# Optimization experiments

Measured on AMD Instinct MI355X. Metric: run time of the kernel, lower is better.

Reference implementation:

```python
import jax, jax.numpy as jnp
import numpy as np

N, D, E = 50000, 128, 640000


def setup_inputs() -> dict:
    key = jax.random.key(0)
    ks = jax.random.split(key, 8)
    x = jax.random.normal(ks[0], (N, D), dtype=jnp.float32)
    coord = jax.random.normal(ks[1], (N, 3), dtype=jnp.float32)
    edge_index = jax.random.randint(ks[2], (2, E), 0, N, dtype=jnp.int64)
    s = 1.0 / np.sqrt(D)
    W_edge = jax.random.normal(ks[3], (1, D), dtype=jnp.float32)
    b_edge = jnp.zeros((D,), dtype=jnp.float32)
    W1 = jax.random.normal(ks[4], (2 * D, D), dtype=jnp.float32) * s
    b1 = jnp.zeros((D,), dtype=jnp.float32)
    W2 = jax.random.normal(ks[5], (D, D), dtype=jnp.float32) * s
    b2 = jnp.zeros((D,), dtype=jnp.float32)
    return {"x": x, "coord": coord, "edge_index": edge_index,
            "W_edge": W_edge, "b_edge": b_edge,
            "W1": W1, "b1": b1, "W2": W2, "b2": b2}


def reference(x, coord, edge_index, W_edge, b_edge, W1, b1, W2, b2):
    row, col = edge_index[0], edge_index[1]
    dx = coord[row] - coord[col]                      # [E, 3]
    dist = jnp.linalg.norm(dx, axis=-1, keepdims=True)  # [E, 1]
    edge_attr = dist @ W_edge + b_edge                # [E, D]
    edge_msg = jnp.concatenate([x[col], edge_attr], axis=-1)  # [E, 2D]
    h = jax.nn.relu(edge_msg @ W1 + b1)               # [E, D]
    msg = h @ W2 + b2                                 # [E, D]
    agg = jax.ops.segment_sum(msg, row, num_segments=x.shape[0])  # [N, D]
    return x + agg
```

## Files before the change

kernel.cpp:

```cpp
#include <hip/hip_runtime.h>
#include <hip/hip_fp16.h>
#include <hip/hip_bf16.h>
#include <math.h>

#define D 128
#define LDAP 136
#define CAP 64
#define OVMAX 1024

typedef unsigned int   u32;
typedef unsigned short u16;
using f32x4 = __attribute__((ext_vector_type(4))) float;
using s16x8 = __attribute__((ext_vector_type(8))) short;
using u32x4 = __attribute__((ext_vector_type(4))) unsigned int;

__device__ __forceinline__ u16 f2bf(float f) {
    u32 u = __float_as_uint(f);
    return (u16)((u + 0x7FFFu + ((u >> 16) & 1u)) >> 16);
}

__device__ __forceinline__ bool detect_is64(const int* __restrict__ idx32, int E) {
    int lane = threadIdx.x & 63;
    int hi = 0;
    if (lane < E) hi = idx32[2 * lane + 1];
    return __ballot(hi != 0) == 0ull;
}

__global__ __launch_bounds__(128) void prep_zero_kernel(
    const float* __restrict__ W_edge, const float* __restrict__ b_edge,
    const float* __restrict__ W1, const float* __restrict__ b1,
    const float* __restrict__ W2, float* __restrict__ wc,
    u16* __restrict__ Wt1, u16* __restrict__ Wt2,
    u32x4* __restrict__ counts4, int nz4, u32* __restrict__ ovCount)
{
    const int b = blockIdx.x, t = threadIdx.x;
    if (b < D) {
        Wt1[b * D + t] = f2bf(W1[(size_t)t * D + b]);
        Wt2[b * D + t] = f2bf(W2[(size_t)t * D + b]);
    } else if (b == D) {
        if (t == 0) *ovCount = 0u;
        float w = 0.f, c = 0.f;
        #pragma unroll 8
        for (int k = 0; k < D; ++k) {
            float w1 = W1[(size_t)(D + k) * D + t];
            w = fmaf(W_edge[k], w1, w);
            c = fmaf(b_edge[k], w1, c);
        }
        wc[t]     = w;
        wc[D + t] = c + b1[t];
    } else {
        int i = (b - D - 1) * 128 + t;
        if (i < nz4) counts4[i] = (u32x4){0u, 0u, 0u, 0u};
    }
}

__global__ __launch_bounds__(256) void count_direct_kernel(
    const void* __restrict__ eidx, const float* __restrict__ coord,
    u32* __restrict__ counts, u32* __restrict__ packed,
    u32* __restrict__ ovCount, u32* __restrict__ ovRow,
    u32* __restrict__ ovRec, int E)
{
    const bool is64 = detect_is64((const int*)eidx, E);
    const long long* e64 = (const long long*)eidx;
    const int*       e32 = (const int*)eidx;
    const int e = blockIdx.x * 256 + threadIdx.x;
    if (e >= E) return;

    int row, col;
    if (is64) { row = (int)e64[e]; col = (int)e64[E + e]; }
    else      { row = e32[e];      col = e32[E + e];      }

    u32 seq = atomicAdd(&counts[row], 1u);

    float dx = coord[3 * row + 0] - coord[3 * col + 0];
    float dy = coord[3 * row + 1] - coord[3 * col + 1];
    float dz = coord[3 * row + 2] - coord[3 * col + 2];
    float dist = sqrtf(fmaf(dx, dx, fmaf(dy, dy, dz * dz)));
    u32 rec = (u32)col | ((u32)__half_as_ushort(__float2half(dist)) << 16);

    if (seq < (u32)CAP) {
        __builtin_nontemporal_store(rec, &packed[((u32)row << 6) + seq]);
    } else {
        u32 k = atomicAdd(ovCount, 1u);
        if (k < (u32)OVMAX) { ovRow[k] = (u32)row; ovRec[k] = rec; }
    }
}

__global__ __launch_bounds__(256) void aggregate_kernel(
    const u16* __restrict__ ybf, const u32* __restrict__ counts,
    const u32* __restrict__ packed, const float* __restrict__ wc,
    u32* __restrict__ Hb2, const u32* __restrict__ ovCount,
    const u32* __restrict__ ovRow, const u32* __restrict__ ovRec, int N)
{
    const int lane = threadIdx.x & 63;
    const int row  = blockIdx.x * 4 + (threadIdx.x >> 6);
    if (row >= N) return;

    const float2 wv = ((const float2*)wc)[lane];
    const float2 cv = ((const float2*)(wc + D))[lane];

    const u32 deg = counts[row];
    const u32 beg = (u32)row << 6;
    const u32 end = beg + (deg < (u32)CAP ? deg : (u32)CAP);
    float a0[4] = {0.f, 0.f, 0.f, 0.f};
    float a1[4] = {0.f, 0.f, 0.f, 0.f};

    for (u32 base = beg; base < end; base += 16) {
        u32 p[16], yv[16];
        #pragma unroll
        for (int j = 0; j < 16; ++j) {
            u32 ee = base + j;
            p[j] = packed[ee < end ? ee : end - 1];
        }
        #pragma unroll
        for (int j = 0; j < 16; ++j)
            yv[j] = *(const u32*)(ybf + (size_t)(p[j] & 0xFFFFu) * D + 2 * lane);
        #pragma unroll
        for (int j = 0; j < 16; ++j) {
            float dt = __half2float(__ushort_as_half((u16)(p[j] >> 16)));
            float v0 = fmaxf(0.f, fmaf(dt, wv.x, __uint_as_float(yv[j] << 16)         + cv.x));
            float v1 = fmaxf(0.f, fmaf(dt, wv.y, __uint_as_float(yv[j] & 0xFFFF0000u) + cv.y));
            bool ok = (base + j) < end;
            a0[j & 3] += ok ? v0 : 0.f;
            a1[j & 3] += ok ? v1 : 0.f;
        }
    }
    if (deg > (u32)CAP) {
        u32 ov = *ovCount; if (ov > (u32)OVMAX) ov = (u32)OVMAX;
        for (u32 i = 0; i < ov; ++i) {
            if (ovRow[i] == (u32)row) {
                u32 pr = ovRec[i];
                float dt = __half2float(__ushort_as_half((u16)(pr >> 16)));
                u32 yv = *(const u32*)(ybf + (size_t)(pr & 0xFFFFu) * D + 2 * lane);
                a0[0] += fmaxf(0.f, fmaf(dt, wv.x, __uint_as_float(yv << 16)         + cv.x));
                a1[0] += fmaxf(0.f, fmaf(dt, wv.y, __uint_as_float(yv & 0xFFFF0000u) + cv.y));
            }
        }
    }
    float r0 = (a0[0] + a0[1]) + (a0[2] + a0[3]);
    float r1 = (a1[0] + a1[1]) + (a1[2] + a1[3]);
    Hb2[(size_t)row * 64 + lane] = (u32)f2bf(r0) | ((u32)f2bf(r1) << 16);
}

template <int AMODE, int EPI>
__global__ __launch_bounds__(256) void mfma_gemm_kernel(
    const void* __restrict__ Asrc, const u16* __restrict__ Wt,
    const float* __restrict__ xres, const u32* __restrict__ degi,
    const float* __restrict__ bvec, void* __restrict__ out, int N)
{
    __shared__ u16 wl[D * LDAP];
    __shared__ u16 al[64 * LDAP];
    const int t    = threadIdx.x;
    const int lane = t & 63;
    const int w    = t >> 6;
    const int n0   = blockIdx.x * 64;

    #pragma unroll
    for (int i = 0; i < 8; ++i) {
        int e = (i * 256 + t) * 8;
        int r = e >> 7, c = e & 127;
        *(u32x4*)&wl[r * LDAP + c] = *(const u32x4*)&Wt[r * D + c];
    }
    if (AMODE == 0) {
        const float* A = (const float*)Asrc;
        #pragma unroll
        for (int i = 0; i < 8; ++i) {
            int idx = i * 256 + t;
            int r = idx >> 5, c4 = idx & 31;
            int gr = n0 + r; if (gr >= N) gr = N - 1;
            float4 v = *(const float4*)&A[(size_t)gr * D + c4 * 4];
            u32 lo = (u32)f2bf(v.x) | ((u32)f2bf(v.y) << 16);
            u32 hi = (u32)f2bf(v.z) | ((u32)f2bf(v.w) << 16);
            *(uint2*)&al[r * LDAP + c4 * 4] = make_uint2(lo, hi);
        }
    } else {
        const u16* A = (const u16*)Asrc;
        #pragma unroll
        for (int i = 0; i < 4; ++i) {
            int idx = i * 256 + t;
            int r = idx >> 4, c8 = idx & 15;
            int gr = n0 + r; if (gr >= N) gr = N - 1;
            *(u32x4*)&al[r * LDAP + c8 * 8] = *(const u32x4*)&A[(size_t)gr * D + c8 * 8];
        }
    }
    __syncthreads();

    const int  fr     = lane & 15;
    const int  kg     = lane >> 4;
    const bool wvalid = (n0 + w * 16) < N;

    f32x4 acc[8];
    #pragma unroll
    for (int i = 0; i < 8; ++i) acc[i] = (f32x4){0.f, 0.f, 0.f, 0.f};

    #pragma unroll
    for (int kk = 0; kk < 4; ++kk) {
        const int ko = kk * 32 + kg * 8;
        s16x8 a = *(const s16x8*)&al[(w * 16 + fr) * LDAP + ko];
        #pragma unroll
        for (int ct = 0; ct < 8; ++ct) {
            s16x8 b = *(const s16x8*)&wl[(ct * 16 + fr) * LDAP + ko];
            acc[ct] = __builtin_amdgcn_mfma_f32_16x16x32_bf16(a, b, acc[ct], 0, 0, 0);
        }
    }

    if (!wvalid) return;

    if (EPI == 0) {
        u16* O = (u16*)out;
        #pragma unroll
        for (int ct = 0; ct < 8; ++ct) {
            const int c = ct * 16 + fr;
            #pragma unroll
            for (int j = 0; j < 4; ++j) {
                int R = n0 + w * 16 + 4 * kg + j;
                O[(size_t)R * D + c] = f2bf(acc[ct][j]);
            }
        }
    } else {
        float* O = (float*)out;
        float degf[4];
        #pragma unroll
        for (int j = 0; j < 4; ++j)
            degf[j] = (float)degi[n0 + w * 16 + 4 * kg + j];
        #pragma unroll
        for (int ct = 0; ct < 8; ++ct) {
            const int c  = ct * 16 + fr;
            const float bv = bvec[c];
            #pragma unroll
            for (int j = 0; j < 4; ++j) {
                int R = n0 + w * 16 + 4 * kg + j;
                float r = acc[ct][j] + xres[(size_t)R * D + c] + degf[j] * bv;
                O[(size_t)R * D + c] = r;
            }
        }
    }
}

extern "C" void kernel_launch(void* const* d_in, const int* in_sizes, int n_in,
                              void* d_out, int out_size, void* d_ws, size_t ws_size,
                              hipStream_t stream)
{
    const float* x      = (const float*)d_in[0];
    const float* coord  = (const float*)d_in[1];
    const void*  eidx   = d_in[2];
    const float* W_edge = (const float*)d_in[3];
    const float* b_edge = (const float*)d_in[4];
    const float* W1     = (const float*)d_in[5];
    const float* b1     = (const float*)d_in[6];
    const float* W2     = (const float*)d_in[7];
    const float* b2     = (const float*)d_in[8];

    const int N = in_sizes[1] / 3;
    const int E = in_sizes[2] / 2;

    char* wsb    = (char*)d_ws;
    u16*  Hb     = (u16*)wsb;                 size_t o = (size_t)N * D * 2;
    u32*  counts = (u32*)(wsb + o);           o += (size_t)(N + 16) * 4;
    float* wc    = (float*)(wsb + o);         o += 2 * D * 4 + 64;
    u16*  Wt1    = (u16*)(wsb + o);           o += D * D * 2;
    u16*  Wt2    = (u16*)(wsb + o);           o += D * D * 2;
    u32*  ovCount = (u32*)(wsb + o);          o += 64;
    u32*  ovRow   = (u32*)(wsb + o);          o += OVMAX * 4;
    u32*  ovRec   = (u32*)(wsb + o);

    char* ob     = (char*)d_out;
    u16*  ybf    = (u16*)ob;
    u32*  packed = (u32*)(ob + (size_t)N * D * 2);

    const int nz4 = (N + 16 + 3) / 4;
    const int ZB  = (nz4 + 127) / 128;
    prep_zero_kernel<<<D + 1 + ZB, 128, 0, stream>>>(
        W_edge, b_edge, W1, b1, W2, wc, Wt1, Wt2, (u32x4*)counts, nz4, ovCount);

    const int CB = (E + 255) / 256;
    count_direct_kernel<<<CB, 256, 0, stream>>>(
        eidx, coord, counts, packed, ovCount, ovRow, ovRec, E);

    const int GB = (N + 63) / 64;
    mfma_gemm_kernel<0, 0><<<GB, 256, 0, stream>>>(
        x, Wt1, nullptr, nullptr, nullptr, (void*)ybf, N);

    aggregate_kernel<<<(N + 3) / 4, 256, 0, stream>>>(
        ybf, counts, packed, wc, (u32*)Hb, ovCount, ovRow, ovRec, N);

    mfma_gemm_kernel<1, 1><<<GB, 256, 0, stream>>>(
        Hb, Wt2, x, counts, b2, d_out, N);
}
```

Baseline: 99.82 us.

## Merge edge-count scatter and first GEMM into one heterogeneous launch

The edge counting/packing kernel and the first node GEMM (x·W1) are independent, so they are merged into one grid where the first CB blocks do the edge scatter and the remaining blocks do the MFMA GEMM. This removes one kernel launch and lets the atomic-heavy scatter overlap with the compute-bound GEMM. The cost is that the scatter blocks now declare the GEMM's large shared-memory arrays, which can lower their occupancy. The packed-record store also changes from a nontemporal store to a plain store.

After: 92.62 us. 7.2% less time.

```diff
diff --git a/kernel.cpp b/kernel.cpp
--- a/kernel.cpp
+++ b/kernel.cpp
@@ -54,35 +54,97 @@
     }
 }
 
-__global__ __launch_bounds__(256) void count_direct_kernel(
+__global__ __launch_bounds__(256) void count_gemm1_kernel(
     const void* __restrict__ eidx, const float* __restrict__ coord,
     u32* __restrict__ counts, u32* __restrict__ packed,
     u32* __restrict__ ovCount, u32* __restrict__ ovRow,
-    u32* __restrict__ ovRec, int E)
-{
-    const bool is64 = detect_is64((const int*)eidx, E);
-    const long long* e64 = (const long long*)eidx;
-    const int*       e32 = (const int*)eidx;
-    const int e = blockIdx.x * 256 + threadIdx.x;
-    if (e >= E) return;
-
-    int row, col;
-    if (is64) { row = (int)e64[e]; col = (int)e64[E + e]; }
-    else      { row = e32[e];      col = e32[E + e];      }
-
-    u32 seq = atomicAdd(&counts[row], 1u);
-
-    float dx = coord[3 * row + 0] - coord[3 * col + 0];
-    float dy = coord[3 * row + 1] - coord[3 * col + 1];
-    float dz = coord[3 * row + 2] - coord[3 * col + 2];
-    float dist = sqrtf(fmaf(dx, dx, fmaf(dy, dy, dz * dz)));
-    u32 rec = (u32)col | ((u32)__half_as_ushort(__float2half(dist)) << 16);
-
-    if (seq < (u32)CAP) {
-        __builtin_nontemporal_store(rec, &packed[((u32)row << 6) + seq]);
-    } else {
-        u32 k = atomicAdd(ovCount, 1u);
-        if (k < (u32)OVMAX) { ovRow[k] = (u32)row; ovRec[k] = rec; }
+    u32* __restrict__ ovRec, int E, int CB,
+    const float* __restrict__ A, const u16* __restrict__ Wt,
+    u16* __restrict__ ybf, int N)
+{
+    __shared__ u16 wl[D * LDAP];
+    __shared__ u16 al[64 * LDAP];
+
+    if ((int)blockIdx.x < CB) {
+        const bool is64 = detect_is64((const int*)eidx, E);
+        const long long* e64 = (const long long*)eidx;
+        const int*       e32 = (const int*)eidx;
+        const int e = blockIdx.x * 256 + threadIdx.x;
+        if (e >= E) return;
+
+        int row, col;
+        if (is64) { row = (int)e64[e]; col = (int)e64[E + e]; }
+        else      { row = e32[e];      col = e32[E + e];      }
+
+        u32 seq = atomicAdd(&counts[row], 1u);
+
+        float dx = coord[3 * row + 0] - coord[3 * col + 0];
+        float dy = coord[3 * row + 1] - coord[3 * col + 1];
+        float dz = coord[3 * row + 2] - coord[3 * col + 2];
+        float dist = sqrtf(fmaf(dx, dx, fmaf(dy, dy, dz * dz)));
+        u32 rec = (u32)col | ((u32)__half_as_ushort(__float2half(dist)) << 16);
+
+        if (seq < (u32)CAP) {
+            packed[((u32)row << 6) + seq] = rec;
+        } else {
+            u32 k = atomicAdd(ovCount, 1u);
+            if (k < (u32)OVMAX) { ovRow[k] = (u32)row; ovRec[k] = rec; }
+        }
+        return;
+    }
+
+    const int bid  = blockIdx.x - CB;
+    const int t    = threadIdx.x;
+    const int lane = t & 63;
+    const int w    = t >> 6;
+    const int n0   = bid * 64;
+
+    #pragma unroll
+    for (int i = 0; i < 8; ++i) {
+        int e = (i * 256 + t) * 8;
+        int r = e >> 7, c = e & 127;
+        *(u32x4*)&wl[r * LDAP + c] = *(const u32x4*)&Wt[r * D + c];
+    }
+    #pragma unroll
+    for (int i = 0; i < 8; ++i) {
+        int idx = i * 256 + t;
+        int r = idx >> 5, c4 = idx & 31;
+        int gr = n0 + r; if (gr >= N) gr = N - 1;
+        float4 v = *(const float4*)&A[(size_t)gr * D + c4 * 4];
+        u32 lo = (u32)f2bf(v.x) | ((u32)f2bf(v.y) << 16);
+        u32 hi = (u32)f2bf(v.z) | ((u32)f2bf(v.w) << 16);
+        *(uint2*)&al[r * LDAP + c4 * 4] = make_uint2(lo, hi);
+    }
+    __syncthreads();
+
+    const int  fr     = lane & 15;
+    const int  kg     = lane >> 4;
+    const bool wvalid = (n0 + w * 16) < N;
+
+    f32x4 acc[8];
+    #pragma unroll
+    for (int i = 0; i < 8; ++i) acc[i] = (f32x4){0.f, 0.f, 0.f, 0.f};
+
+    #pragma unroll
+    for (int kk = 0; kk < 4; ++kk) {
+        const int ko = kk * 32 + kg * 8;
+        s16x8 a = *(const s16x8*)&al[(w * 16 + fr) * LDAP + ko];
+        #pragma unroll
+        for (int ct = 0; ct < 8; ++ct) {
+            s16x8 b = *(const s16x8*)&wl[(ct * 16 + fr) * LDAP + ko];
+            acc[ct] = __builtin_amdgcn_mfma_f32_16x16x32_bf16(a, b, acc[ct], 0, 0, 0);
+        }
+    }
+    if (!wvalid) return;
+
+    #pragma unroll
+    for (int ct = 0; ct < 8; ++ct) {
+        const int c = ct * 16 + fr;
+        #pragma unroll
+        for (int j = 0; j < 4; ++j) {
+            int R = n0 + w * 16 + 4 * kg + j;
+            ybf[(size_t)R * D + c] = f2bf(acc[ct][j]);
+        }
     }
 }
 
@@ -142,11 +204,10 @@
     Hb2[(size_t)row * 64 + lane] = (u32)f2bf(r0) | ((u32)f2bf(r1) << 16);
 }
 
-template <int AMODE, int EPI>
-__global__ __launch_bounds__(256) void mfma_gemm_kernel(
-    const void* __restrict__ Asrc, const u16* __restrict__ Wt,
+__global__ __launch_bounds__(256) void gemm2_kernel(
+    const u16* __restrict__ Asrc, const u16* __restrict__ Wt,
     const float* __restrict__ xres, const u32* __restrict__ degi,
-    const float* __restrict__ bvec, void* __restrict__ out, int N)
+    const float* __restrict__ bvec, float* __restrict__ out, int N)
 {
     __shared__ u16 wl[D * LDAP];
     __shared__ u16 al[64 * LDAP];
@@ -161,27 +222,12 @@
         int r = e >> 7, c = e & 127;
         *(u32x4*)&wl[r * LDAP + c] = *(const u32x4*)&Wt[r * D + c];
     }
-    if (AMODE == 0) {
-        const float* A = (const float*)Asrc;
-        #pragma unroll
-        for (int i = 0; i < 8; ++i) {
-            int idx = i * 256 + t;
-            int r = idx >> 5, c4 = idx & 31;
-            int gr = n0 + r; if (gr >= N) gr = N - 1;
-            float4 v = *(const float4*)&A[(size_t)gr * D + c4 * 4];
-            u32 lo = (u32)f2bf(v.x) | ((u32)f2bf(v.y) << 16);
-            u32 hi = (u32)f2bf(v.z) | ((u32)f2bf(v.w) << 16);
-            *(uint2*)&al[r * LDAP + c4 * 4] = make_uint2(lo, hi);
-        }
-    } else {
-        const u16* A = (const u16*)Asrc;
-        #pragma unroll
-        for (int i = 0; i < 4; ++i) {
-            int idx = i * 256 + t;
-            int r = idx >> 4, c8 = idx & 15;
-            int gr = n0 + r; if (gr >= N) gr = N - 1;
-            *(u32x4*)&al[r * LDAP + c8 * 8] = *(const u32x4*)&A[(size_t)gr * D + c8 * 8];
-        }
+    #pragma unroll
+    for (int i = 0; i < 4; ++i) {
+        int idx = i * 256 + t;
+        int r = idx >> 4, c8 = idx & 15;
+        int gr = n0 + r; if (gr >= N) gr = N - 1;
+        *(u32x4*)&al[r * LDAP + c8 * 8] = *(const u32x4*)&Asrc[(size_t)gr * D + c8 * 8];
     }
     __syncthreads();
 
@@ -203,36 +249,21 @@
             acc[ct] = __builtin_amdgcn_mfma_f32_16x16x32_bf16(a, b, acc[ct], 0, 0, 0);
         }
     }
-
     if (!wvalid) return;
 
-    if (EPI == 0) {
-        u16* O = (u16*)out;
-        #pragma unroll
-        for (int ct = 0; ct < 8; ++ct) {
-            const int c = ct * 16 + fr;
-            #pragma unroll
-            for (int j = 0; j < 4; ++j) {
-                int R = n0 + w * 16 + 4 * kg + j;
-                O[(size_t)R * D + c] = f2bf(acc[ct][j]);
-            }
-        }
-    } else {
-        float* O = (float*)out;
-        float degf[4];
-        #pragma unroll
-        for (int j = 0; j < 4; ++j)
-            degf[j] = (float)degi[n0 + w * 16 + 4 * kg + j];
-        #pragma unroll
-        for (int ct = 0; ct < 8; ++ct) {
-            const int c  = ct * 16 + fr;
-            const float bv = bvec[c];
-            #pragma unroll
-            for (int j = 0; j < 4; ++j) {
-                int R = n0 + w * 16 + 4 * kg + j;
-                float r = acc[ct][j] + xres[(size_t)R * D + c] + degf[j] * bv;
-                O[(size_t)R * D + c] = r;
-            }
+    float degf[4];
+    #pragma unroll
+    for (int j = 0; j < 4; ++j)
+        degf[j] = (float)degi[n0 + w * 16 + 4 * kg + j];
+    #pragma unroll
+    for (int ct = 0; ct < 8; ++ct) {
+        const int c  = ct * 16 + fr;
+        const float bv = bvec[c];
+        #pragma unroll
+        for (int j = 0; j < 4; ++j) {
+            int R = n0 + w * 16 + 4 * kg + j;
+            float r = acc[ct][j] + xres[(size_t)R * D + c] + degf[j] * bv;
+            out[(size_t)R * D + c] = r;
         }
     }
 }
@@ -274,16 +305,14 @@
         W_edge, b_edge, W1, b1, W2, wc, Wt1, Wt2, (u32x4*)counts, nz4, ovCount);
 
     const int CB = (E + 255) / 256;
-    count_direct_kernel<<<CB, 256, 0, stream>>>(
-        eidx, coord, counts, packed, ovCount, ovRow, ovRec, E);
-
     const int GB = (N + 63) / 64;
-    mfma_gemm_kernel<0, 0><<<GB, 256, 0, stream>>>(
-        x, Wt1, nullptr, nullptr, nullptr, (void*)ybf, N);
+    count_gemm1_kernel<<<CB + GB, 256, 0, stream>>>(
+        eidx, coord, counts, packed, ovCount, ovRow, ovRec, E, CB,
+        x, Wt1, ybf, N);
 
     aggregate_kernel<<<(N + 3) / 4, 256, 0, stream>>>(
         ybf, counts, packed, wc, (u32*)Hb, ovCount, ovRow, ovRec, N);
 
-    mfma_gemm_kernel<1, 1><<<GB, 256, 0, stream>>>(
-        Hb, Wt2, x, counts, b2, d_out, N);
-}
+    gemm2_kernel<<<GB, 256, 0, stream>>>(
+        Hb, Wt2, x, counts, b2, (float*)d_out, N);
+}
```
